# Optimization experiments

Measured on AMD Instinct MI355X. Metric: run time of the kernel, lower is better.

The kernel has to match this reference:

```python
import jax, jax.numpy as jnp
import numpy as np

B, S, H, G, W = 4, 4096, 1024, 256, 8
CHUNK = 1024
NUM_HEADS = 4


def _ln(x, g, b, eps=1e-5):
    m = jnp.mean(x, axis=-1, keepdims=True)
    v = jnp.var(x, axis=-1, keepdims=True)
    return (x - m) / jnp.sqrt(v + eps) * g + b


def setup_inputs() -> dict:
    key = jax.random.key(0)
    ks = jax.random.split(key, 16)
    Hm = H // 2
    return {
        "x": jax.random.normal(ks[0], (B, S, H), dtype=jnp.float32),
        # wavelet params
        "mother_wavelets": jax.random.normal(ks[1], (1, W, H, 1), dtype=jnp.float32) * 0.02,
        "scales": jnp.ones((1, W, 1, 1), dtype=jnp.float32),
        # coeff_mixer: Linear(W,H/2) -> LN -> GELU -> Linear(H/2,H)  (weights stored as (in,out))
        "mix_w1": jax.random.normal(ks[2], (W, Hm), dtype=jnp.float32) * 0.02,
        "mix_b1": jnp.zeros((Hm,), dtype=jnp.float32),
        "mix_ln_g": jnp.ones((Hm,), dtype=jnp.float32),
        "mix_ln_b": jnp.zeros((Hm,), dtype=jnp.float32),
        "mix_w2": jax.random.normal(ks[3], (Hm, H), dtype=jnp.float32) * 0.02,
        "mix_b2": jnp.zeros((H,), dtype=jnp.float32),
        # attention (no bias)
        "wq": jax.random.normal(ks[4], (H, H), dtype=jnp.float32) * 0.02,
        "wk": jax.random.normal(ks[5], (H, H), dtype=jnp.float32) * 0.02,
        "wv": jax.random.normal(ks[6], (H, H), dtype=jnp.float32) * 0.02,
        "wo": jax.random.normal(ks[7], (H, H), dtype=jnp.float32) * 0.02,
        # output_proj: LN -> Linear(H, G)
        "out_ln_g": jnp.ones((H,), dtype=jnp.float32),
        "out_ln_b": jnp.zeros((H,), dtype=jnp.float32),
        "out_w": jax.random.normal(ks[8], (H, G), dtype=jnp.float32) * 0.02,
        "out_b": jnp.zeros((G,), dtype=jnp.float32),
    }


def reference(x, mother_wavelets, scales, mix_w1, mix_b1, mix_ln_g, mix_ln_b,
              mix_w2, mix_b2, wq, wk, wv, wo, out_ln_g, out_ln_b, out_w, out_b):
    b, s, h = x.shape
    nc = s // CHUNK  # chunks are independent -> fold into batch
    xc = x.reshape(b * nc, CHUNK, h)

    # wavelet coeffs: conv1d with kernel length == channels reduces to a dot product
    norm = jnp.sqrt(jnp.sum(mother_wavelets ** 2, axis=2, keepdims=True))
    kern = (mother_wavelets / jnp.maximum(norm, 1e-12)) * jax.nn.sigmoid(scales)
    kern = kern[0, :, :, 0]  # (W, H)
    coeffs = jnp.einsum('bsh,wh->bsw', xc, kern)  # (b*nc, L, W)

    # coeff mixer
    hid = _ln(coeffs @ mix_w1 + mix_b1, mix_ln_g, mix_ln_b)
    mixed = jax.nn.gelu(hid, approximate=False) @ mix_w2 + mix_b2  # (b*nc, L, H)

    # multi-head attention within each chunk (eval mode -> no causal mask)
    hd = h // NUM_HEADS
    def heads(t):
        return t.reshape(-1, CHUNK, NUM_HEADS, hd).transpose(0, 2, 1, 3)
    q, k, v = heads(mixed @ wq), heads(mixed @ wk), heads(mixed @ wv)
    scores = jnp.einsum('bhqd,bhkd->bhqk', q, k) * (hd ** -0.5)
    attn = jax.nn.softmax(scores, axis=-1)
    o = jnp.einsum('bhqk,bhkd->bhqd', attn, v)
    o = o.transpose(0, 2, 1, 3).reshape(-1, CHUNK, h) @ wo

    # output projection with residual
    y = _ln(o + mixed, out_ln_g, out_ln_b) @ out_w + out_b  # (b*nc, L, G)
    return y.reshape(b, s, -1)
```

## Files before the change

### kernel.cpp

```cpp
#include <hip/hip_runtime.h>
#include <hip/hip_bf16.h>

typedef __bf16 bf16;
typedef __bf16 bf16x8 __attribute__((ext_vector_type(8)));
typedef float f32x4 __attribute__((ext_vector_type(4)));
typedef unsigned short ushort8_t __attribute__((ext_vector_type(8)));

#define GLOAD_LDS16(g, l)                                                      \
    __builtin_amdgcn_global_load_lds(                                          \
        (const __attribute__((address_space(1))) void*)(g),                    \
        (__attribute__((address_space(3))) void*)(l), 16, 0, 0)


__global__ __launch_bounds__(256) void k_wavelet(const float* __restrict__ mw,
                                                 const float* __restrict__ sc,
                                                 float* __restrict__ kern) {
    int w = blockIdx.x;
    int tid = threadIdx.x;
    float s = 0.f;
    for (int h = tid; h < 1024; h += 256) { float v = mw[w * 1024 + h]; s += v * v; }
#pragma unroll
    for (int xm = 1; xm < 64; xm <<= 1) s += __shfl_xor(s, xm);
    __shared__ float red[4];
    if ((tid & 63) == 0) red[tid >> 6] = s;
    __syncthreads();
    float tot = red[0] + red[1] + red[2] + red[3];
    float inv = 1.f / fmaxf(sqrtf(tot), 1e-12f);
    float sg = 1.f / (1.f + __expf(-sc[w]));
    float m = inv * sg;
    for (int h = tid; h < 1024; h += 256) kern[w * 1024 + h] = mw[w * 1024 + h] * m;
}

__global__ __launch_bounds__(256) void k_coeffs(const float* __restrict__ x,
                                                const float* __restrict__ kern,
                                                float* __restrict__ coeffs) {
    __shared__ float kl[8 * 1024];
    int tid = threadIdx.x;
    for (int i = tid; i < 8192; i += 256) kl[i] = kern[i];
    __syncthreads();
    int wid = tid >> 6, lane = tid & 63;
    long row = (long)blockIdx.x * 4 + wid;
    float acc[8] = {0, 0, 0, 0, 0, 0, 0, 0};
    const float* xr = x + row * 1024;
    for (int i = 0; i < 16; i++) {
        float xv = xr[lane + i * 64];
#pragma unroll
        for (int w = 0; w < 8; w++) acc[w] += xv * kl[w * 1024 + lane + i * 64];
    }
#pragma unroll
    for (int xm = 1; xm < 64; xm <<= 1) {
#pragma unroll
        for (int w = 0; w < 8; w++) acc[w] += __shfl_xor(acc[w], xm);
    }
    if (lane == 0) {
#pragma unroll
        for (int w = 0; w < 8; w++) coeffs[row * 8 + w] = acc[w];
    }
}

__global__ __launch_bounds__(256) void k_mix1(const float* __restrict__ coeffs,
                                              const float* __restrict__ w1,
                                              const float* __restrict__ b1,
                                              const float* __restrict__ lng,
                                              const float* __restrict__ lnb,
                                              bf16* __restrict__ g) {
    long row = blockIdx.x;
    int tid = threadIdx.x;
    int wid = tid >> 6, lane = tid & 63;
    __shared__ float cf[8];
    __shared__ float red1[4], red2[4];
    if (tid < 8) cf[tid] = coeffs[row * 8 + tid];
    __syncthreads();
    float h0[2];
#pragma unroll
    for (int t = 0; t < 2; t++) {
        int j = tid + t * 256;
        float a = b1[j];
#pragma unroll
        for (int w = 0; w < 8; w++) a += cf[w] * w1[w * 512 + j];
        h0[t] = a;
    }
    float s1 = h0[0] + h0[1];
    float s2 = h0[0] * h0[0] + h0[1] * h0[1];
#pragma unroll
    for (int xm = 1; xm < 64; xm <<= 1) {
        s1 += __shfl_xor(s1, xm);
        s2 += __shfl_xor(s2, xm);
    }
    if (lane == 0) { red1[wid] = s1; red2[wid] = s2; }
    __syncthreads();
    s1 = red1[0] + red1[1] + red1[2] + red1[3];
    s2 = red2[0] + red2[1] + red2[2] + red2[3];
    float mean = s1 * (1.f / 512.f);
    float var = s2 * (1.f / 512.f) - mean * mean;
    float inv = rsqrtf(var + 1e-5f);
#pragma unroll
    for (int t = 0; t < 2; t++) {
        int j = tid + t * 256;
        float xn = (h0[t] - mean) * inv * lng[j] + lnb[j];
        float ge = 0.5f * xn * (1.f + erff(xn * 0.70710678118654752f));
        g[row * 512 + j] = (bf16)ge;
    }
}

__global__ void k_wtrans(const float* __restrict__ w, bf16* __restrict__ wt, int K, int N) {
    long idx = (long)blockIdx.x * 256 + threadIdx.x;
    if (idx < (long)K * N) {
        int kk = (int)(idx / N);
        int n = (int)(idx % N);
        wt[(long)n * K + kk] = (bf16)w[idx];
    }
}

enum { EPI_BF16 = 0, EPI_BF16_BIAS = 1, EPI_F32_BIAS = 2, EPI_VT = 3, EPI_F32 = 4 };

template <int EPI>
__global__ __launch_bounds__(512, 2) void k_gemm256(const bf16* __restrict__ A,
                                                    const bf16* __restrict__ Bt,
                                                    const float* __restrict__ bias,
                                                    void* __restrict__ Cout,
                                                    int K, int lda, int ldb, int ldc,
                                                    float scale) {
    __shared__ bf16 As[2 * 256 * 64];
    __shared__ bf16 Bs[2 * 256 * 64];
    int tid = threadIdx.x;
    int wid = tid >> 6, lane = tid & 63;
    int wr = wid >> 2, wc = wid & 3;
    long m0 = (long)blockIdx.y * 256, n0 = (long)blockIdx.x * 256;
    f32x4 acc[8][4] = {};
    const int lr = lane & 15, ko = (lane >> 4) << 3;

    const int grow = wid * 8 + (lane >> 3);
    const int gcol = (lane & 7) << 3;
    const bf16* aS = A + (m0 + grow) * lda + gcol;
    const bf16* bS = Bt + (n0 + grow) * ldb + gcol;
    bf16* lA = As + wid * 512;
    bf16* lB = Bs + wid * 512;

    const int nt = K >> 6;
#pragma unroll
    for (int i = 0; i < 4; i++) {
        GLOAD_LDS16(aS + (long)(i * 64) * lda, lA + i * 4096);
        GLOAD_LDS16(bS + (long)(i * 64) * ldb, lB + i * 4096);
    }
    __syncthreads();
    int buf = 0;
    for (int t = 0; t < nt; t++) {
        if (t + 1 < nt) {
            const int k0 = (t + 1) << 6;
            const int ob = (buf ^ 1) << 14;
#pragma unroll
            for (int i = 0; i < 4; i++) {
                GLOAD_LDS16(aS + (long)(i * 64) * lda + k0, lA + ob + i * 4096);
                GLOAD_LDS16(bS + (long)(i * 64) * ldb + k0, lB + ob + i * 4096);
            }
        }
        const bf16* At = As + (buf << 14);
        const bf16* Bb = Bs + (buf << 14);
#pragma unroll
        for (int kk = 0; kk < 2; kk++) {
            bf16x8 af[8], bfr[4];
#pragma unroll
            for (int i = 0; i < 8; i++)
                af[i] = *(const bf16x8*)&At[(wr * 128 + i * 16 + lr) * 64 + kk * 32 + ko];
#pragma unroll
            for (int j = 0; j < 4; j++)
                bfr[j] = *(const bf16x8*)&Bb[(wc * 64 + j * 16 + lr) * 64 + kk * 32 + ko];
#pragma unroll
            for (int i = 0; i < 8; i++) {
#pragma unroll
                for (int j = 0; j < 4; j++)
                    acc[i][j] = __builtin_amdgcn_mfma_f32_16x16x32_bf16(af[i], bfr[j], acc[i][j], 0, 0, 0);
            }
        }
        __syncthreads();
        buf ^= 1;
    }
    const int r0 = (lane >> 4) << 2;
#pragma unroll
    for (int i = 0; i < 8; i++) {
#pragma unroll
        for (int j = 0; j < 4; j++) {
#pragma unroll
            for (int e = 0; e < 4; e++) {
                long m = m0 + wr * 128 + i * 16 + r0 + e;
                long n = n0 + wc * 64 + j * 16 + lr;
                float v = acc[i][j][e] * scale;
                if constexpr (EPI == EPI_BF16_BIAS || EPI == EPI_F32_BIAS) v += bias[n];
                if constexpr (EPI == EPI_F32_BIAS || EPI == EPI_F32) {
                    ((float*)Cout)[m * ldc + n] = v;
                } else if constexpr (EPI == EPI_VT) {
                    long c = m >> 10, s = m & 1023, h = n >> 8, d = n & 255;
                    ((bf16*)Cout)[(((c << 2) + h) << 18) + (d << 10) + s] = (bf16)v;
                } else {
                    ((bf16*)Cout)[m * ldc + n] = (bf16)v;
                }
            }
        }
    }
}

template <int EPI>
__global__ __launch_bounds__(256) void k_gemm(const bf16* __restrict__ A,
                                              const bf16* __restrict__ Bt,
                                              const float* __restrict__ bias,
                                              void* __restrict__ Cout,
                                              int M, int N, int K,
                                              int lda, int ldb, int ldc, float scale) {
    __shared__ bf16 As[128 * 32];
    __shared__ bf16 Bs[128 * 32];
    int tid = threadIdx.x;
    int wid = tid >> 6, lane = tid & 63;
    int wr = wid >> 1, wc = wid & 1;
    long m0 = (long)blockIdx.y * 128, n0 = (long)blockIdx.x * 128;
    f32x4 acc[4][4] = {};
    const int lr = lane & 15, ko = (lane >> 4) << 3;

    const int srow = wid * 32 + (lane >> 2);
    const int scol = (lane & 3) << 3;
    const bf16* a0 = A + (m0 + srow) * lda + scol;
    const bf16* a1 = A + (m0 + srow + 16) * lda + scol;
    const bf16* b0 = Bt + (n0 + srow) * ldb + scol;
    const bf16* b1 = Bt + (n0 + srow + 16) * ldb + scol;
    bf16* la0 = As + wid * 1024;
    bf16* la1 = As + wid * 1024 + 512;
    bf16* lb0 = Bs + wid * 1024;
    bf16* lb1 = Bs + wid * 1024 + 512;

    for (int k0 = 0; k0 < K; k0 += 32) {
        GLOAD_LDS16(a0 + k0, la0);
        GLOAD_LDS16(a1 + k0, la1);
        GLOAD_LDS16(b0 + k0, lb0);
        GLOAD_LDS16(b1 + k0, lb1);
        __syncthreads();
        bf16x8 af[4], bfr[4];
#pragma unroll
        for (int i = 0; i < 4; i++)
            af[i] = *(const bf16x8*)&As[(wr * 64 + i * 16 + lr) * 32 + ko];
#pragma unroll
        for (int i = 0; i < 4; i++)
            bfr[i] = *(const bf16x8*)&Bs[(wc * 64 + i * 16 + lr) * 32 + ko];
#pragma unroll
        for (int i = 0; i < 4; i++) {
#pragma unroll
            for (int j = 0; j < 4; j++)
                acc[i][j] = __builtin_amdgcn_mfma_f32_16x16x32_bf16(af[i], bfr[j], acc[i][j], 0, 0, 0);
        }
        __syncthreads();
    }
    const int r0 = (lane >> 4) << 2;
#pragma unroll
    for (int i = 0; i < 4; i++) {
#pragma unroll
        for (int j = 0; j < 4; j++) {
#pragma unroll
            for (int e = 0; e < 4; e++) {
                long m = m0 + wr * 64 + i * 16 + r0 + e;
                long n = n0 + wc * 64 + j * 16 + lr;
                float v = acc[i][j][e] * scale;
                if constexpr (EPI == EPI_BF16_BIAS || EPI == EPI_F32_BIAS) v += bias[n];
                if constexpr (EPI == EPI_F32_BIAS || EPI == EPI_F32) {
                    ((float*)Cout)[m * ldc + n] = v;
                } else if constexpr (EPI == EPI_VT) {
                    long c = m >> 10, s = m & 1023, h = n >> 8, d = n & 255;
                    ((bf16*)Cout)[(((c << 2) + h) << 18) + (d << 10) + s] = (bf16)v;
                } else {
                    ((bf16*)Cout)[m * ldc + n] = (bf16)v;
                }
            }
        }
    }
}

__global__ __launch_bounds__(512, 2) void k_attn(const bf16* __restrict__ q,
                                                 const bf16* __restrict__ k,
                                                 const bf16* __restrict__ vt,
                                                 bf16* __restrict__ ao) {
    __shared__ __align__(16) bf16 smem[2 * 16384 + 2 * 16384 + 8192];
    bf16* Ks = smem;
    bf16* Vs = smem + 32768;
    bf16* Ps = smem + 65536;
    int tid = threadIdx.x;
    int wid = tid >> 6, lane = tid & 63;
    int c = blockIdx.x, h = blockIdx.y, q0 = blockIdx.z * 128;
    const int lr = lane & 15, gq = lane >> 4, ko = gq << 3;
    const int l7 = lr & 7;

    const int krw = wid * 2 + (lane >> 5);
    const int kg = (lane & 31) ^ (krw & 7);
    const bf16* ksrc = k + ((long)c << 10) * 1024 + h * 256 + kg * 8;
    const int vrw = wid * 8 + ((lane >> 3) & 7);
    const int vg = (lane & 7) ^ ((lane >> 3) & 7);
    const bf16* vsrc = vt + ((long)(c * 4 + h) << 18) + vg * 8;

    long qrow = ((long)c << 10) + q0 + wid * 16 + lr;
    bf16x8 qf[8];
#pragma unroll
    for (int kk = 0; kk < 8; kk++)
        qf[kk] = *(const bf16x8*)&q[qrow * 1024 + h * 256 + kk * 32 + ko];

    f32x4 oacc[16] = {};
    float m_run[4] = {-1e30f, -1e30f, -1e30f, -1e30f};
    float l_run[4] = {0.f, 0.f, 0.f, 0.f};

#pragma unroll
    for (int i = 0; i < 4; i++) {
        GLOAD_LDS16(ksrc + (long)(i * 16 + krw) * 1024, Ks + i * 4096 + wid * 512);
        GLOAD_LDS16(vsrc + (long)(i * 64 + vrw) * 1024, Vs + i * 4096 + wid * 512);
    }
    __syncthreads();
    int buf = 0;
    for (int t = 0; t < 16; t++) {
        if (t < 15) {
            const int kb = (t + 1) << 6;
            const int ob = (buf ^ 1) << 14;
#pragma unroll
            for (int i = 0; i < 4; i++) {
                GLOAD_LDS16(ksrc + (long)(kb + i * 16 + krw) * 1024, Ks + ob + i * 4096 + wid * 512);
                GLOAD_LDS16(vsrc + (long)(i * 64 + vrw) * 1024 + kb, Vs + ob + i * 4096 + wid * 512);
            }
        }
        const bf16* Kc = Ks + (buf << 14);
        const bf16* Vc = Vs + (buf << 14);
        f32x4 s[4] = {};
        __builtin_amdgcn_s_setprio(1);
#pragma unroll
        for (int kk = 0; kk < 8; kk++) {
#pragma unroll
            for (int n = 0; n < 4; n++)
                s[n] = __builtin_amdgcn_mfma_f32_16x16x32_bf16(
                    qf[kk],
                    *(const bf16x8*)&Kc[((n * 16 + lr) << 8) + ((((kk << 2) + gq) ^ l7) << 3)],
                    s[n], 0, 0, 0);
        }
        __builtin_amdgcn_s_setprio(0);
        float mx[4], al[4], rs[4];
#pragma unroll
        for (int e = 0; e < 4; e++)
            mx[e] = fmaxf(fmaxf(s[0][e], s[1][e]), fmaxf(s[2][e], s[3][e]));
#pragma unroll
        for (int xm = 1; xm < 16; xm <<= 1) {
#pragma unroll
            for (int e = 0; e < 4; e++) mx[e] = fmaxf(mx[e], __shfl_xor(mx[e], xm));
        }
#pragma unroll
        for (int e = 0; e < 4; e++) {
            float mn = fmaxf(m_run[e], mx[e]);
            al[e] = __expf(m_run[e] - mn);
            m_run[e] = mn;
            rs[e] = 0.f;
        }
#pragma unroll
        for (int n = 0; n < 4; n++) {
#pragma unroll
            for (int e = 0; e < 4; e++) {
                float p = __expf(s[n][e] - m_run[e]);
                s[n][e] = p;
                rs[e] += p;
            }
        }
#pragma unroll
        for (int xm = 1; xm < 16; xm <<= 1) {
#pragma unroll
            for (int e = 0; e < 4; e++) rs[e] += __shfl_xor(rs[e], xm);
        }
#pragma unroll
        for (int e = 0; e < 4; e++) l_run[e] = l_run[e] * al[e] + rs[e];
#pragma unroll
        for (int f = 0; f < 16; f++) {
#pragma unroll
            for (int e = 0; e < 4; e++) oacc[f][e] *= al[e];
        }
#pragma unroll
        for (int n = 0; n < 4; n++) {
#pragma unroll
            for (int e = 0; e < 4; e++) {
                const int rw = (gq << 2) + e;
                Ps[(wid << 10) + (rw << 6) + ((((n << 1) + (lr >> 3)) ^ (rw & 7)) << 3) + (lr & 7)] =
                    (bf16)s[n][e];
            }
        }
        const int pg = gq ^ l7;
        bf16x8 pf0 = *(const bf16x8*)&Ps[(wid << 10) + (lr << 6) + (pg << 3)];
        bf16x8 pf1 = *(const bf16x8*)&Ps[(wid << 10) + (lr << 6) + ((pg ^ 4) << 3)];
        __builtin_amdgcn_s_setprio(1);
#pragma unroll
        for (int n2 = 0; n2 < 16; n2++) {
            const int vrow = (n2 * 16 + lr) << 6;
            const int vswz = gq ^ l7;
            oacc[n2] = __builtin_amdgcn_mfma_f32_16x16x32_bf16(
                pf0, *(const bf16x8*)&Vc[vrow + (vswz << 3)], oacc[n2], 0, 0, 0);
            oacc[n2] = __builtin_amdgcn_mfma_f32_16x16x32_bf16(
                pf1, *(const bf16x8*)&Vc[vrow + ((vswz ^ 4) << 3)], oacc[n2], 0, 0, 0);
        }
        __builtin_amdgcn_s_setprio(0);
        __syncthreads();
        buf ^= 1;
    }
#pragma unroll
    for (int n2 = 0; n2 < 16; n2++) {
#pragma unroll
        for (int e = 0; e < 4; e++) {
            long row = ((long)c << 10) + q0 + wid * 16 + (gq << 2) + e;
            long col = ((long)h << 8) + n2 * 16 + lr;
            ao[row * 1024 + col] = (bf16)(oacc[n2][e] / l_run[e]);
        }
    }
}

__global__ __launch_bounds__(256) void k_outln(const float* __restrict__ o,
                                               const bf16* __restrict__ mixed,
                                               const float* __restrict__ g,
                                               const float* __restrict__ b,
                                               bf16* __restrict__ t) {
    long row = blockIdx.x;
    int tid = threadIdx.x;
    int wid = tid >> 6, lane = tid & 63;
    __shared__ float red1[4], red2[4];
    float x[4];
    const float* orow = o + row * 1024;
    const bf16* mrow = mixed + row * 1024;
#pragma unroll
    for (int i = 0; i < 4; i++) {
        int j = tid * 4 + i;
        x[i] = orow[j] + (float)mrow[j];
    }
    float s1 = x[0] + x[1] + x[2] + x[3];
    float s2 = x[0] * x[0] + x[1] * x[1] + x[2] * x[2] + x[3] * x[3];
#pragma unroll
    for (int xm = 1; xm < 64; xm <<= 1) {
        s1 += __shfl_xor(s1, xm);
        s2 += __shfl_xor(s2, xm);
    }
    if (lane == 0) { red1[wid] = s1; red2[wid] = s2; }
    __syncthreads();
    s1 = red1[0] + red1[1] + red1[2] + red1[3];
    s2 = red2[0] + red2[1] + red2[2] + red2[3];
    float mean = s1 * (1.f / 1024.f);
    float var = s2 * (1.f / 1024.f) - mean * mean;
    float inv = rsqrtf(var + 1e-5f);
#pragma unroll
    for (int i = 0; i < 4; i++) {
        int j = tid * 4 + i;
        t[row * 1024 + j] = (bf16)((x[i] - mean) * inv * g[j] + b[j]);
    }
}

extern "C" void kernel_launch(void* const* d_in, const int* in_sizes, int n_in,
                              void* d_out, int out_size, void* d_ws, size_t ws_size,
                              hipStream_t stream) {
    const float* x   = (const float*)d_in[0];
    const float* mw  = (const float*)d_in[1];
    const float* sc  = (const float*)d_in[2];
    const float* w1  = (const float*)d_in[3];
    const float* b1  = (const float*)d_in[4];
    const float* lng1 = (const float*)d_in[5];
    const float* lnb1 = (const float*)d_in[6];
    const float* w2  = (const float*)d_in[7];
    const float* b2  = (const float*)d_in[8];
    const float* wq  = (const float*)d_in[9];
    const float* wk  = (const float*)d_in[10];
    const float* wv  = (const float*)d_in[11];
    const float* wo  = (const float*)d_in[12];
    const float* lng2 = (const float*)d_in[13];
    const float* lnb2 = (const float*)d_in[14];
    const float* ow  = (const float*)d_in[15];
    const float* ob  = (const float*)d_in[16];

    char* p = (char*)d_ws;
    auto take = [&](size_t bytes) {
        char* r = p;
        p += (bytes + 255) & ~(size_t)255;
        return r;
    };
    const size_t M = 16384;
    float* kern   = (float*)take(8 * 1024 * sizeof(float));
    float* coeffs = (float*)take(M * 8 * sizeof(float));
    bf16* g       = (bf16*)take(M * 512 * 2);
    bf16* mixed   = (bf16*)take(M * 1024 * 2);
    bf16* qb      = (bf16*)take(M * 1024 * 2 * 2);
    bf16* kb2     = qb + M * 1024;
    float* o32    = (float*)qb;
    bf16* vtb     = (bf16*)take(M * 1024 * 2);
    bf16* tb      = vtb;
    bf16* aob     = (bf16*)take(M * 1024 * 2);
    bf16* w2t     = (bf16*)take((size_t)1024 * 512 * 2);
    bf16* wqt     = (bf16*)take((size_t)1024 * 1024 * 2);
    bf16* wkt     = (bf16*)take((size_t)1024 * 1024 * 2);
    bf16* wvt     = (bf16*)take((size_t)1024 * 1024 * 2);
    bf16* wot     = (bf16*)take((size_t)1024 * 1024 * 2);
    bf16* owt     = (bf16*)take((size_t)256 * 1024 * 2);

    k_wavelet<<<8, 256, 0, stream>>>(mw, sc, kern);
    k_coeffs<<<4096, 256, 0, stream>>>(x, kern, coeffs);
    k_mix1<<<16384, 256, 0, stream>>>(coeffs, w1, b1, lng1, lnb1, g);

    k_wtrans<<<(512 * 1024) / 256, 256, 0, stream>>>(w2, w2t, 512, 1024);
    k_wtrans<<<(1024 * 1024) / 256, 256, 0, stream>>>(wq, wqt, 1024, 1024);
    k_wtrans<<<(1024 * 1024) / 256, 256, 0, stream>>>(wk, wkt, 1024, 1024);
    k_wtrans<<<(1024 * 1024) / 256, 256, 0, stream>>>(wv, wvt, 1024, 1024);
    k_wtrans<<<(1024 * 1024) / 256, 256, 0, stream>>>(wo, wot, 1024, 1024);
    k_wtrans<<<(1024 * 256) / 256, 256, 0, stream>>>(ow, owt, 1024, 256);

    k_gemm256<EPI_BF16_BIAS><<<dim3(4, 64), 512, 0, stream>>>(
        g, w2t, b2, mixed, 512, 512, 512, 1024, 1.f);
    k_gemm256<EPI_BF16><<<dim3(4, 64), 512, 0, stream>>>(
        mixed, wqt, nullptr, qb, 1024, 1024, 1024, 1024, 0.0625f);
    k_gemm256<EPI_BF16><<<dim3(4, 64), 512, 0, stream>>>(
        mixed, wkt, nullptr, kb2, 1024, 1024, 1024, 1024, 1.f);
    k_gemm256<EPI_VT><<<dim3(4, 64), 512, 0, stream>>>(
        mixed, wvt, nullptr, vtb, 1024, 1024, 1024, 1024, 1.f);
    k_attn<<<dim3(16, 4, 8), 512, 0, stream>>>(qb, kb2, vtb, aob);
    k_gemm256<EPI_F32><<<dim3(4, 64), 512, 0, stream>>>(
        aob, wot, nullptr, o32, 1024, 1024, 1024, 1024, 1.f);
    k_outln<<<16384, 256, 0, stream>>>(o32, mixed, lng2, lnb2, tb);
    k_gemm<EPI_F32_BIAS><<<dim3(2, 128), 256, 0, stream>>>(
        tb, owt, ob, d_out, 16384, 256, 1024, 1024, 1024, 256, 1.f);
}
```

Measured before the change: 476.8 us.

## Use lazy softmax rescaling and transposed LDS reads for the P fragment

The flash-attention loop now rescales the output accumulators and running sum only when some row's new max exceeds the running max by more than 8, checked wave-wide with __any. This skips most of the 64 accumulator multiplies and exps per tile. P is now written to LDS as packed bf16x4 vectors and read back with ds_read_b64_tr_b16 transposing loads, replacing 16 scalar swizzled stores. The lazy threshold lets unnormalised exponentials grow up to e^8 before rescaling, and the inline asm waitcnts and sched_barrier limit how the compiler can overlap this section.

```diff
diff --git a/kernel.cpp b/kernel.cpp
--- a/kernel.cpp
+++ b/kernel.cpp
@@ -2,14 +2,18 @@
 #include <hip/hip_bf16.h>
 
 typedef __bf16 bf16;
+typedef __bf16 bf16x4 __attribute__((ext_vector_type(4)));
 typedef __bf16 bf16x8 __attribute__((ext_vector_type(8)));
 typedef float f32x4 __attribute__((ext_vector_type(4)));
 typedef unsigned short ushort8_t __attribute__((ext_vector_type(8)));
+typedef unsigned int u32x2 __attribute__((ext_vector_type(2)));
 
 #define GLOAD_LDS16(g, l)                                                      \
     __builtin_amdgcn_global_load_lds(                                          \
         (const __attribute__((address_space(1))) void*)(g),                    \
         (__attribute__((address_space(3))) void*)(l), 16, 0, 0)
+
+#define LDS_ADDR(p) ((unsigned)(uintptr_t)(__attribute__((address_space(3))) void*)(p))
 
 
 __global__ __launch_bounds__(256) void k_wavelet(const float* __restrict__ mw,
@@ -303,6 +307,9 @@
     float m_run[4] = {-1e30f, -1e30f, -1e30f, -1e30f};
     float l_run[4] = {0.f, 0.f, 0.f, 0.f};
 
+    bf16* PT = Ps + (wid << 10);
+    const unsigned pva = LDS_ADDR(&PT[(gq << 7) + lr]);
+
 #pragma unroll
     for (int i = 0; i < 4; i++) {
         GLOAD_LDS16(ksrc + (long)(i * 16 + krw) * 1024, Ks + i * 4096 + wid * 512);
@@ -334,7 +341,7 @@
                     s[n], 0, 0, 0);
         }
         __builtin_amdgcn_s_setprio(0);
-        float mx[4], al[4], rs[4];
+        float mx[4];
 #pragma unroll
         for (int e = 0; e < 4; e++)
             mx[e] = fmaxf(fmaxf(s[0][e], s[1][e]), fmaxf(s[2][e], s[3][e]));
@@ -343,13 +350,20 @@
 #pragma unroll
             for (int e = 0; e < 4; e++) mx[e] = fmaxf(mx[e], __shfl_xor(mx[e], xm));
         }
-#pragma unroll
-        for (int e = 0; e < 4; e++) {
-            float mn = fmaxf(m_run[e], mx[e]);
-            al[e] = __expf(m_run[e] - mn);
-            m_run[e] = mn;
-            rs[e] = 0.f;
-        }
+        bool need = (mx[0] > m_run[0] + 8.f) || (mx[1] > m_run[1] + 8.f) ||
+                    (mx[2] > m_run[2] + 8.f) || (mx[3] > m_run[3] + 8.f);
+        if (__any(need)) {
+#pragma unroll
+            for (int e = 0; e < 4; e++) {
+                float mn = fmaxf(m_run[e], mx[e]);
+                float al = __expf(m_run[e] - mn);
+                m_run[e] = mn;
+                l_run[e] *= al;
+#pragma unroll
+                for (int f = 0; f < 16; f++) oacc[f][e] *= al;
+            }
+        }
+        float rs[4] = {0.f, 0.f, 0.f, 0.f};
 #pragma unroll
         for (int n = 0; n < 4; n++) {
 #pragma unroll
@@ -365,24 +379,24 @@
             for (int e = 0; e < 4; e++) rs[e] += __shfl_xor(rs[e], xm);
         }
 #pragma unroll
-        for (int e = 0; e < 4; e++) l_run[e] = l_run[e] * al[e] + rs[e];
-#pragma unroll
-        for (int f = 0; f < 16; f++) {
-#pragma unroll
-            for (int e = 0; e < 4; e++) oacc[f][e] *= al[e];
-        }
+        for (int e = 0; e < 4; e++) l_run[e] += rs[e];
 #pragma unroll
         for (int n = 0; n < 4; n++) {
-#pragma unroll
-            for (int e = 0; e < 4; e++) {
-                const int rw = (gq << 2) + e;
-                Ps[(wid << 10) + (rw << 6) + ((((n << 1) + (lr >> 3)) ^ (rw & 7)) << 3) + (lr & 7)] =
-                    (bf16)s[n][e];
-            }
-        }
-        const int pg = gq ^ l7;
-        bf16x8 pf0 = *(const bf16x8*)&Ps[(wid << 10) + (lr << 6) + (pg << 3)];
-        bf16x8 pf1 = *(const bf16x8*)&Ps[(wid << 10) + (lr << 6) + ((pg ^ 4) << 3)];
+            bf16x4 pv = {(bf16)s[n][0], (bf16)s[n][1], (bf16)s[n][2], (bf16)s[n][3]};
+            *(bf16x4*)&PT[((n * 16 + lr) << 4) + (gq << 2)] = pv;
+        }
+        asm volatile("s_waitcnt lgkmcnt(0)" ::: "memory");
+        u32x2 t0, t1, t2, t3;
+        asm volatile("ds_read_b64_tr_b16 %0, %1" : "=v"(t0) : "v"(pva));
+        asm volatile("ds_read_b64_tr_b16 %0, %1 offset:128" : "=v"(t1) : "v"(pva));
+        asm volatile("ds_read_b64_tr_b16 %0, %1 offset:1024" : "=v"(t2) : "v"(pva));
+        asm volatile("ds_read_b64_tr_b16 %0, %1 offset:1152" : "=v"(t3) : "v"(pva));
+        asm volatile("s_waitcnt lgkmcnt(0)" ::: "memory");
+        __builtin_amdgcn_sched_barrier(0);
+        union { u32x2 u[2]; bf16x8 v; } p0, p1;
+        p0.u[0] = t0; p0.u[1] = t1;
+        p1.u[0] = t2; p1.u[1] = t3;
+        const bf16x8 pf0 = p0.v, pf1 = p1.v;
         __builtin_amdgcn_s_setprio(1);
 #pragma unroll
         for (int n2 = 0; n2 < 16; n2++) {
```

Result: no change. 477.4 us (+0.1%).
